# Kernel optimization log

Measured on AMD Instinct MI355X. Metric: run time of the kernel, lower is better.

Reference implementation:

```python
import jax, jax.numpy as jnp
import numpy as np

THETA_BASE = 10000.0


def rope(x):
    # x: [B, S, D], D even. Interleaved-pair rotary embedding.
    B, S, D = x.shape
    pos = jnp.arange(S, dtype=jnp.float32)                       # [S]
    p = jnp.arange(D // 2, dtype=jnp.float32)                    # p-1 in the torch code
    inv_freq = 1.0 / (THETA_BASE ** (2.0 * p / D))               # [D/2]
    theta = pos[:, None] * inv_freq[None, :]                     # [S, D/2]
    sin_t, cos_t = jnp.sin(theta), jnp.cos(theta)
    x1 = x[..., 0::2]                                            # [B, S, D/2]
    x2 = x[..., 1::2]
    r1 = x1 * cos_t - x2 * sin_t
    r2 = x1 * sin_t + x2 * cos_t
    return jnp.stack((r1, r2), axis=-1).reshape(B, S, D)


def setup_inputs() -> dict:
    key = jax.random.key(0)
    k_x, k_q, k_k, k_v = jax.random.split(key, 4)
    B, S, E, DH = 4, 4096, 1024, 64
    x = jax.random.normal(k_x, (B, S, E), dtype=jnp.float32)
    # causal lower-triangular mask (mask==0 positions are disallowed)
    mask = jnp.tril(jnp.ones((S, S), dtype=jnp.int32))
    W_Q = jax.random.uniform(k_q, (E, DH), dtype=jnp.float32)
    W_K = jax.random.uniform(k_k, (E, DH), dtype=jnp.float32)
    W_V = jax.random.uniform(k_v, (E, DH), dtype=jnp.float32)
    return {"x": x, "mask": mask, "W_Q": W_Q, "W_K": W_K, "W_V": W_V}


def reference(x, mask, W_Q, W_K, W_V):
    d_h = W_Q.shape[1]
    Q = x @ W_Q                                                  # [B, S, d_h]
    K = x @ W_K
    V = x @ W_V
    Q, K = rope(Q), rope(K)
    scores = jnp.einsum('bqd,bkd->bqk', Q, K) / jnp.sqrt(jnp.float32(d_h))
    masked = jnp.where(mask == 0, -jnp.inf, scores)              # broadcast [S,S] -> [B,S,S]
    attn = jax.nn.softmax(masked, axis=-1)
    return jnp.einsum('bqk,bkd->bqd', attn, V)
```

## Files before the change

kernel.cpp:

```cpp
#include <hip/hip_runtime.h>

typedef short short8  __attribute__((ext_vector_type(8)));
typedef short short4v __attribute__((ext_vector_type(4)));
typedef float f32x4   __attribute__((ext_vector_type(4)));

#define NB 4
#define NS 4096
#define NE 1024
#define ND 64

__device__ __forceinline__ short f2bf(float f) {
    unsigned u = __builtin_bit_cast(unsigned, f);
    u = (u + 0x7FFFu + ((u >> 16) & 1u)) >> 16;
    return (short)u;
}
__device__ __forceinline__ float bf2f(short s) {
    unsigned u = ((unsigned)(unsigned short)s) << 16;
    return __builtin_bit_cast(float, u);
}

__global__ void prep_wt(const float* __restrict__ WQ, const float* __restrict__ WK,
                        const float* __restrict__ WV,
                        short* __restrict__ wtp_hi, short* __restrict__ wtp_lo) {
    int idx = blockIdx.x * 256 + threadIdx.x;
    if (idx >= 192 * NE) return;
    int n = idx >> 10, k = idx & (NE - 1);
    int sel = n >> 6, d = n & 63;
    const float* W = (sel == 0) ? WQ : (sel == 1 ? WK : WV);
    float v = W[k * ND + d];
    if (sel == 0) v *= 0.125f;
    short hi = f2bf(v);
    short lo = f2bf(v - bf2f(hi));
    int off = ((k >> 5) * 12 + (n >> 4)) * 512 + ((k & 31) >> 3) * 128 + (n & 15) * 8 + (k & 7);
    wtp_hi[off] = hi;
    wtp_lo[off] = lo;
}

__global__ __launch_bounds__(256, 2) void proj_rope(
        const float* __restrict__ x,
        const short* __restrict__ wtp_hi, const short* __restrict__ wtp_lo,
        short* __restrict__ qhi, short* __restrict__ qlo,
        short* __restrict__ kfph, short* __restrict__ kfpl,
        short* __restrict__ vfp) {
    __shared__ short Xh[32 * 64], Xl[32 * 64];
    const int tid = threadIdx.x;
    const int w = tid >> 6, lane = tid & 63;
    const int g = lane >> 4, cl = lane & 15;
    const int rb = blockIdx.x << 5;
    const int c0 = w * 48;

    f32x4 acc[2][3];
    #pragma unroll
    for (int i = 0; i < 2; ++i)
        #pragma unroll
        for (int j = 0; j < 3; ++j) acc[i][j] = (f32x4){0.f, 0.f, 0.f, 0.f};

    const int srow = tid >> 3, skc = tid & 7;
    const float* xs0 = x + (size_t)(rb + srow) * NE + (skc << 3);
    const int swoff = srow * 64 + ((skc ^ (srow & 7)) << 3);

    const short* bph = wtp_hi + (size_t)(c0 >> 4) * 512 + (lane << 3);
    const short* bpl = wtp_lo + (size_t)(c0 >> 4) * 512 + (lane << 3);

    float4 xr0, xr1;
    short8 b0[6], b1[6];

#define LOADXR(kk) { xr0 = *(const float4*)(xs0 + (kk)); \
                     xr1 = *(const float4*)(xs0 + (kk) + 4); }
#define LOADB(Bs, kk) {                                                      \
        const int ko = ((kk) >> 5) * 6144;                                   \
        _Pragma("unroll")                                                    \
        for (int ct = 0; ct < 3; ++ct) {                                     \
            Bs[ct * 2]     = *(const short8*)(bph + ko + ct * 512);          \
            Bs[ct * 2 + 1] = *(const short8*)(bpl + ko + ct * 512);          \
        } }
#define HALF(h, Bs) {                                                        \
        _Pragma("unroll")                                                    \
        for (int rt = 0; rt < 2; ++rt) {                                     \
            const int R = (rt << 4) + cl;                                    \
            const int ro = R * 64 + ((((h) * 4 + g) ^ (R & 7)) << 3);        \
            short8 ah = *(const short8*)(Xh + ro);                           \
            short8 al = *(const short8*)(Xl + ro);                           \
            _Pragma("unroll")                                                \
            for (int ct = 0; ct < 3; ++ct) {                                 \
                acc[rt][ct] = __builtin_amdgcn_mfma_f32_16x16x32_bf16(ah, Bs[ct*2],   acc[rt][ct], 0, 0, 0); \
                acc[rt][ct] = __builtin_amdgcn_mfma_f32_16x16x32_bf16(ah, Bs[ct*2+1], acc[rt][ct], 0, 0, 0); \
                acc[rt][ct] = __builtin_amdgcn_mfma_f32_16x16x32_bf16(al, Bs[ct*2],   acc[rt][ct], 0, 0, 0); \
            }                                                                \
        } }

    LOADXR(0);
    LOADB(b0, 0);

    #pragma unroll 1
    for (int k0 = 0; k0 < NE; k0 += 64) {
        short8 h8, l8;
        {
            float vv[8] = {xr0.x, xr0.y, xr0.z, xr0.w, xr1.x, xr1.y, xr1.z, xr1.w};
            #pragma unroll
            for (int q = 0; q < 8; ++q) {
                short h = f2bf(vv[q]);
                h8[q] = h;
                l8[q] = f2bf(vv[q] - bf2f(h));
            }
        }
        __syncthreads();
        *(short8*)(Xh + swoff) = h8;
        *(short8*)(Xl + swoff) = l8;
        if (k0 + 64 < NE) LOADXR(k0 + 64);
        LOADB(b1, k0 + 32);
        __syncthreads();
        HALF(0, b0);
        if (k0 + 64 < NE) LOADB(b0, k0 + 64);
        HALF(1, b1);
    }
#undef LOADXR
#undef LOADB
#undef HALF

    #pragma unroll
    for (int rt = 0; rt < 2; ++rt) {
        #pragma unroll
        for (int ct = 0; ct < 3; ++ct) {
            int c = c0 + (ct << 4) + cl;
            #pragma unroll
            for (int r = 0; r < 4; ++r) {
                int row = rb + (rt << 4) + (g << 2) + r;
                int s = row & (NS - 1);
                int b = row >> 12;
                float val = acc[rt][ct][r];
                if (c < 128) {
                    int d = c & 63;
                    int p = d >> 1;
                    float freq = exp2f(-(float)p * 0.41524101186091903f);
                    float theta = (float)s * freq;
                    float sn = sinf(theta), cs = cosf(theta);
                    float partner = __shfl_xor(val, 1);
                    float rot = (c & 1) ? fmaf(partner, sn, val * cs)
                                        : fmaf(-partner, sn, val * cs);
                    short hi = f2bf(rot);
                    short lo = f2bf(rot - bf2f(hi));
                    if (c < 64) {
                        int off = row * ND + d;
                        qhi[off] = hi; qlo[off] = lo;
                    } else {
                        int off = ((b << 7) + (s >> 5)) * 2048 + ((s >> 4) & 1) * 1024
                                + (d >> 5) * 512 + (((d >> 3) & 3) * 16 + (s & 15)) * 8 + (d & 7);
                        kfph[off] = hi; kfpl[off] = lo;
                    }
                } else {
                    int d = c - 128;
                    int off = ((b << 7) + (s >> 5)) * 2048 + (d >> 4) * 512
                            + (((s >> 3) & 3) * 16 + (d & 15)) * 8 + (s & 7);
                    vfp[off] = f2bf(val);
                }
            }
        }
    }
}

__global__ __launch_bounds__(256, 4) void attn_fused(
        const short* __restrict__ qhi, const short* __restrict__ qlo,
        const short* __restrict__ kfph, const short* __restrict__ kfpl,
        const short* __restrict__ vfp, float* __restrict__ outp) {
    __shared__ short Ps[4][16][40];
    __shared__ float Co[4][16][66];
    __shared__ float Cm[4][16], Cls[4][16];
    const int tid = threadIdx.x;
    const int lane = tid & 63, w = tid >> 6;
    const int g = lane >> 4, cl = lane & 15;
    const int bid = blockIdx.x;
    const int b = (bid >> 1) & 3;
    const int t = 255 - (((bid >> 3) << 1) | (bid & 1));
    const int qw = t << 4;
    const int rowb = b << 12;

    short8 qh[2], ql[2];
    #pragma unroll
    for (int ks = 0; ks < 2; ++ks) {
        int off = ((rowb + qw + cl) << 6) + (ks << 5) + (g << 3);
        qh[ks] = *(const short8*)(qhi + off);
        ql[ks] = *(const short8*)(qlo + off);
    }

    f32x4 o[4];
    #pragma unroll
    for (int i = 0; i < 4; ++i) o[i] = (f32x4){0.f, 0.f, 0.f, 0.f};
    float m = -1e38f, lsp = 0.f;

    const int nkv = (t >> 1) + 1;
    const short* kbaseh = kfph + (size_t)(b << 7) * 2048 + (lane << 3);
    const short* kbasel = kfpl + (size_t)(b << 7) * 2048 + (lane << 3);
    const short* vbase  = vfp  + (size_t)(b << 7) * 2048 + (lane << 3);

    short8 kf[2][4];
    short8 vf[4];

#define LOADK(jj) {                                                          \
        _Pragma("unroll")                                                    \
        for (int ci = 0; ci < 2; ++ci) {                                     \
            const short* kh = kbaseh + (jj) * 2048 + ci * 1024;              \
            const short* kl = kbasel + (jj) * 2048 + ci * 1024;              \
            kf[ci][0] = *(const short8*)(kh);                                \
            kf[ci][1] = *(const short8*)(kh + 512);                          \
            kf[ci][2] = *(const short8*)(kl);                                \
            kf[ci][3] = *(const short8*)(kl + 512);                          \
        } }
#define LOADV(jj) {                                                          \
        _Pragma("unroll")                                                    \
        for (int dt = 0; dt < 4; ++dt)                                       \
            vf[dt] = *(const short8*)(vbase + (jj) * 2048 + dt * 512);       \
        }

    if (w < nkv) {
        LOADK(w); LOADV(w);
        #pragma unroll 1
        for (int j = w; j < nkv; j += 4) {
            f32x4 sc[2];
            #pragma unroll
            for (int ci = 0; ci < 2; ++ci) {
                f32x4 s = (f32x4){0.f, 0.f, 0.f, 0.f};
                s = __builtin_amdgcn_mfma_f32_16x16x32_bf16(kf[ci][0], qh[0], s, 0, 0, 0);
                s = __builtin_amdgcn_mfma_f32_16x16x32_bf16(kf[ci][1], qh[1], s, 0, 0, 0);
                s = __builtin_amdgcn_mfma_f32_16x16x32_bf16(kf[ci][0], ql[0], s, 0, 0, 0);
                s = __builtin_amdgcn_mfma_f32_16x16x32_bf16(kf[ci][1], ql[1], s, 0, 0, 0);
                s = __builtin_amdgcn_mfma_f32_16x16x32_bf16(kf[ci][2], qh[0], s, 0, 0, 0);
                s = __builtin_amdgcn_mfma_f32_16x16x32_bf16(kf[ci][3], qh[1], s, 0, 0, 0);
                sc[ci] = s;
            }
            const int jn = j + 4;
            if (jn < nkv) LOADK(jn);

            if (j == nkv - 1) {
                #pragma unroll
                for (int ci = 0; ci < 2; ++ci)
                    #pragma unroll
                    for (int r = 0; r < 4; ++r)
                        if ((j << 5) + (ci << 4) + (g << 2) + r > qw + cl) sc[ci][r] = -1e30f;
            }
            float pm = fmaxf(fmaxf(fmaxf(sc[0][0], sc[0][1]), fmaxf(sc[0][2], sc[0][3])),
                             fmaxf(fmaxf(sc[1][0], sc[1][1]), fmaxf(sc[1][2], sc[1][3])));
            pm = fmaxf(pm, __shfl_xor(pm, 16));
            pm = fmaxf(pm, __shfl_xor(pm, 32));
            const float mo = m;
            m = fmaxf(m, pm);
            const float rs = __expf(mo - m);
            float psum = 0.f;
            #pragma unroll
            for (int ci = 0; ci < 2; ++ci) {
                float p0 = __expf(sc[ci][0] - m), p1 = __expf(sc[ci][1] - m);
                float p2 = __expf(sc[ci][2] - m), p3 = __expf(sc[ci][3] - m);
                psum += (p0 + p1) + (p2 + p3);
                short4v pk;
                pk[0] = f2bf(p0); pk[1] = f2bf(p1); pk[2] = f2bf(p2); pk[3] = f2bf(p3);
                *(short4v*)(&Ps[w][cl][(ci << 4) + (g << 2)]) = pk;
            }
            lsp = lsp * rs + psum;
            if (__any(m > mo)) {
                float rs4[4];
                #pragma unroll
                for (int r = 0; r < 4; ++r) rs4[r] = __shfl(rs, (g << 2) + r);
                #pragma unroll
                for (int dt = 0; dt < 4; ++dt)
                    #pragma unroll
                    for (int r = 0; r < 4; ++r) o[dt][r] *= rs4[r];
            }
            short8 pa = *(short8*)(&Ps[w][cl][g << 3]);
            #pragma unroll
            for (int dt = 0; dt < 4; ++dt)
                o[dt] = __builtin_amdgcn_mfma_f32_16x16x32_bf16(pa, vf[dt], o[dt], 0, 0, 0);
            if (jn < nkv) LOADV(jn);
        }
    }
#undef LOADK
#undef LOADV

    lsp += __shfl_xor(lsp, 16);
    lsp += __shfl_xor(lsp, 32);
    if (g == 0) { Cm[w][cl] = m; Cls[w][cl] = lsp; }
    #pragma unroll
    for (int dt = 0; dt < 4; ++dt)
        #pragma unroll
        for (int r = 0; r < 4; ++r)
            Co[w][(g << 2) + r][(dt << 4) + cl] = o[dt][r];
    __syncthreads();

    if (w == 0) {
        #pragma unroll
        for (int r = 0; r < 4; ++r) {
            const int row = (g << 2) + r;
            float M = fmaxf(fmaxf(Cm[0][row], Cm[1][row]), fmaxf(Cm[2][row], Cm[3][row]));
            float e0 = __expf(Cm[0][row] - M), e1 = __expf(Cm[1][row] - M);
            float e2 = __expf(Cm[2][row] - M), e3 = __expf(Cm[3][row] - M);
            float L = Cls[0][row] * e0 + Cls[1][row] * e1 + Cls[2][row] * e2 + Cls[3][row] * e3;
            float inv = 1.f / L;
            #pragma unroll
            for (int dt = 0; dt < 4; ++dt) {
                int d = (dt << 4) + cl;
                float O = Co[0][row][d] * e0 + Co[1][row][d] * e1
                        + Co[2][row][d] * e2 + Co[3][row][d] * e3;
                outp[(rowb + qw + row) * ND + d] = O * inv;
            }
        }
    }
}

extern "C" void kernel_launch(void* const* d_in, const int* in_sizes, int n_in,
                              void* d_out, int out_size, void* d_ws, size_t ws_size,
                              hipStream_t stream) {
    const float* x  = (const float*)d_in[0];
    const float* WQ = (const float*)d_in[2];
    const float* WK = (const float*)d_in[3];
    const float* WV = (const float*)d_in[4];

    const size_t need = 786432u + 5u * 2097152u;
    if (ws_size < need) return;

    char* ws = (char*)d_ws;
    short* wtph = (short*)(ws);
    short* wtpl = (short*)(ws + 393216);
    short* qhi  = (short*)(ws + 786432);
    short* qlo  = (short*)(ws + 786432 + 1 * 2097152);
    short* kfph = (short*)(ws + 786432 + 2 * 2097152);
    short* kfpl = (short*)(ws + 786432 + 3 * 2097152);
    short* vfp  = (short*)(ws + 786432 + 4 * 2097152);

    prep_wt<<<768, 256, 0, stream>>>(WQ, WK, WV, wtph, wtpl);
    proj_rope<<<512, 256, 0, stream>>>(x, wtph, wtpl, qhi, qlo, kfph, kfpl, vfp);
    attn_fused<<<1024, 256, 0, stream>>>(qhi, qlo, kfph, kfpl, vfp, (float*)d_out);
}
```

Measured before the change: 81.26 us.

## Write K/V row-major from projection and repack into fragment layout in separate kernel

The projection epilogue now writes K in plain row-major order and V in a simpler per-32-row transposed tile, so the scattered 2-byte stores become more contiguous. A new kv_pack kernel stages each 2048-element tile in shared memory and rewrites it in place into the fragment layout the attention kernel expects. This is meant to cut the cost of the scattered global stores, at the price of an extra kernel launch and another read/write pass over K and V.

```diff
diff --git a/kernel.cpp b/kernel.cpp
--- a/kernel.cpp
+++ b/kernel.cpp
@@ -40,8 +40,8 @@
         const float* __restrict__ x,
         const short* __restrict__ wtp_hi, const short* __restrict__ wtp_lo,
         short* __restrict__ qhi, short* __restrict__ qlo,
-        short* __restrict__ kfph, short* __restrict__ kfpl,
-        short* __restrict__ vfp) {
+        short* __restrict__ khi, short* __restrict__ klo,
+        short* __restrict__ vtb) {
     __shared__ short Xh[32 * 64], Xl[32 * 64];
     const int tid = threadIdx.x;
     const int w = tid >> 6, lane = tid & 63;
@@ -140,23 +140,38 @@
                                         : fmaf(-partner, sn, val * cs);
                     short hi = f2bf(rot);
                     short lo = f2bf(rot - bf2f(hi));
-                    if (c < 64) {
-                        int off = row * ND + d;
-                        qhi[off] = hi; qlo[off] = lo;
-                    } else {
-                        int off = ((b << 7) + (s >> 5)) * 2048 + ((s >> 4) & 1) * 1024
-                                + (d >> 5) * 512 + (((d >> 3) & 3) * 16 + (s & 15)) * 8 + (d & 7);
-                        kfph[off] = hi; kfpl[off] = lo;
-                    }
+                    int off = row * ND + d;
+                    if (c < 64) { qhi[off] = hi; qlo[off] = lo; }
+                    else        { khi[off] = hi; klo[off] = lo; }
                 } else {
                     int d = c - 128;
-                    int off = ((b << 7) + (s >> 5)) * 2048 + (d >> 4) * 512
-                            + (((s >> 3) & 3) * 16 + (d & 15)) * 8 + (s & 7);
-                    vfp[off] = f2bf(val);
+                    vtb[(b << 18) + ((s >> 5) << 11) + (d << 5) + (s & 31)] = f2bf(val);
                 }
             }
         }
     }
+}
+
+__global__ __launch_bounds__(256) void kv_pack(short* __restrict__ khi,
+                                               short* __restrict__ klo,
+                                               short* __restrict__ vtb) {
+    __shared__ short Xh[2048], Xl[2048], Vl[2048];
+    const int tid = threadIdx.x;
+    const size_t base = (size_t)blockIdx.x * 2048;
+    *(short8*)(Xh + tid * 8) = *(const short8*)(khi + base + tid * 8);
+    *(short8*)(Xl + tid * 8) = *(const short8*)(klo + base + tid * 8);
+    *(short8*)(Vl + tid * 8) = *(const short8*)(vtb + base + tid * 8);
+    __syncthreads();
+    const int ci = (tid >> 7) & 1, hf = (tid >> 6) & 1, ln = tid & 63;
+    const int srcK = (ci * 16 + (ln & 15)) * 64 + hf * 32 + (ln >> 4) * 8;
+    short8 okh = *(const short8*)(Xh + srcK);
+    short8 okl = *(const short8*)(Xl + srcK);
+    const int dt = (tid >> 6) & 3;
+    const int srcV = (dt * 16 + (ln & 15)) * 32 + (ln >> 4) * 8;
+    short8 ov = *(const short8*)(Vl + srcV);
+    *(short8*)(khi + base + tid * 8) = okh;
+    *(short8*)(klo + base + tid * 8) = okl;
+    *(short8*)(vtb + base + tid * 8) = ov;
 }
 
 __global__ __launch_bounds__(256, 4) void attn_fused(
@@ -321,11 +336,12 @@
     short* wtpl = (short*)(ws + 393216);
     short* qhi  = (short*)(ws + 786432);
     short* qlo  = (short*)(ws + 786432 + 1 * 2097152);
-    short* kfph = (short*)(ws + 786432 + 2 * 2097152);
-    short* kfpl = (short*)(ws + 786432 + 3 * 2097152);
-    short* vfp  = (short*)(ws + 786432 + 4 * 2097152);
+    short* khi  = (short*)(ws + 786432 + 2 * 2097152);
+    short* klo  = (short*)(ws + 786432 + 3 * 2097152);
+    short* vtb  = (short*)(ws + 786432 + 4 * 2097152);
 
     prep_wt<<<768, 256, 0, stream>>>(WQ, WK, WV, wtph, wtpl);
-    proj_rope<<<512, 256, 0, stream>>>(x, wtph, wtpl, qhi, qlo, kfph, kfpl, vfp);
-    attn_fused<<<1024, 256, 0, stream>>>(qhi, qlo, kfph, kfpl, vfp, (float*)d_out);
-}
+    proj_rope<<<512, 256, 0, stream>>>(x, wtph, wtpl, qhi, qlo, khi, klo, vtb);
+    kv_pack<<<512, 256, 0, stream>>>(khi, klo, vtb);
+    attn_fused<<<1024, 256, 0, stream>>>(qhi, qlo, khi, klo, vtb, (float*)d_out);
+}
```

Result: no change. 82.09 us (+1.0%).
